# Kernel tuning notes

Measured on AMD Instinct MI355X. Metric: run time of the kernel, lower is better.

The kernel has to match this reference:

```python
import jax, jax.numpy as jnp
import numpy as np

K = 512          # patch size
H = 16           # heads
C = 768          # dim
ROPE_BASE = 100.0
COUNTS = [8000, 8300, 7800, 8668]


def _build_pad_unpad(counts, k):
    # faithful numpy replica of EfficientAttentionV2.get_padding_and_inverse
    counts = np.asarray(counts, dtype=np.int64)
    cpad = np.where(counts > k, ((counts + k - 1) // k) * k, counts)
    off = np.concatenate([[0], np.cumsum(counts)])
    offp = np.concatenate([[0], np.cumsum(cpad)])
    pad = np.arange(offp[-1])
    unpad = np.arange(off[-1])
    for i in range(len(counts)):
        unpad[off[i]:off[i + 1]] += offp[i] - off[i]
        if counts[i] != cpad[i]:
            s = offp[i + 1] - k + counts[i] % k
            pad[s:offp[i + 1]] = pad[s - k:offp[i + 1] - k]
        pad[offp[i]:offp[i + 1]] -= offp[i] - off[i]
    return pad, unpad


def setup_inputs() -> dict:
    key = jax.random.key(0)
    ks = jax.random.split(key, 6)
    N = int(np.sum(COUNTS))
    pad, unpad = _build_pad_unpad(COUNTS, K)
    rng = np.random.default_rng(0)
    perm = rng.permutation(N)                 # serialized_order stand-in
    inv_perm = np.argsort(perm)               # serialized_inverse
    order = perm[pad].astype(np.int32)        # [N_pad]
    inverse = unpad[inv_perm].astype(np.int32)  # [N]
    grid = rng.integers(0, 1024, size=(N, 3))
    pos = grid[order].astype(np.int32)        # [N_pad, 3], gathered grid coords
    s = 0.02
    return {
        "x": jax.random.normal(ks[0], (N, C), jnp.float32),
        "w_qkv": jax.random.normal(ks[1], (C, 3 * C), jnp.float32) * s,
        "b_qkv": jnp.zeros((3 * C,), jnp.float32),
        "w_proj": jax.random.normal(ks[2], (C, C), jnp.float32) * s,
        "b_proj": jnp.zeros((C,), jnp.float32),
        "order": jnp.asarray(order),
        "inverse": jnp.asarray(inverse),
        "pos": jnp.asarray(pos),
    }


def _rope1d(tok, pos1d):
    # tok: [P, K, H, d], pos1d: [P, K]
    d = tok.shape[-1]
    inv_freq = 1.0 / (ROPE_BASE ** (jnp.arange(0, d, 2, dtype=jnp.float32) / d))
    fr = pos1d[..., None].astype(jnp.float32) * inv_freq      # [P, K, d/2]
    fr = jnp.concatenate([fr, fr], axis=-1)[:, :, None, :]    # [P, K, 1, d]
    x1, x2 = jnp.split(tok, 2, axis=-1)
    rot = jnp.concatenate([-x2, x1], axis=-1)
    return tok * jnp.cos(fr) + rot * jnp.sin(fr)


def _rope3d(tok, pos):
    # tok: [P, K, H, D]; pos: [P, K, 3]; split head dim into 3 axis chunks
    parts = jnp.split(tok, 3, axis=-1)
    return jnp.concatenate(
        [_rope1d(parts[i], pos[..., i]) for i in range(3)], axis=-1)


def reference(x, w_qkv, b_qkv, w_proj, b_proj, order, inverse, pos):
    D = C // H
    scale = D ** -0.5
    qkv = x @ w_qkv + b_qkv                     # [N, 3C]
    qkv = qkv[order]                            # [N_pad, 3C] patch gather
    qkv = qkv.reshape(-1, K, 3, H, D)           # [P, K, 3, H, D]
    q, k, v = qkv[:, :, 0], qkv[:, :, 1], qkv[:, :, 2]  # [P, K, H, D]
    ppos = pos.reshape(-1, K, 3)
    q = _rope3d(q, ppos)
    k = _rope3d(k, ppos)
    attn = jnp.einsum("pkhd,pmhd->phkm", q, k) * scale
    attn = jax.nn.softmax(attn, axis=-1)
    feat = jnp.einsum("phkm,pmhd->pkhd", attn, v).reshape(-1, C)  # [N_pad, C]
    feat = feat[inverse]                        # [N, C] scatter-back
    return feat @ w_proj + b_proj
```

## Files before the change

### kernel.cpp

```cpp
#include <hip/hip_runtime.h>
#include <hip/hip_bf16.h>
#include <stdint.h>

typedef short short8 __attribute__((ext_vector_type(8)));
typedef short short4v __attribute__((ext_vector_type(4)));
typedef float f32x4 __attribute__((ext_vector_type(4)));
typedef float f32x16 __attribute__((ext_vector_type(16)));

#define AS1C(p) ((const __attribute__((address_space(1))) unsigned int*)(p))
#define AS3(p)  ((__attribute__((address_space(3))) unsigned int*)(p))

__device__ __forceinline__ short f2bf(float f) {
  union { float f; unsigned u; } v; v.f = f;
  unsigned r = v.u + 0x7FFFu + ((v.u >> 16) & 1u);
  return (short)(r >> 16);
}

__global__ void k_cast_bf16(const float* __restrict__ src, short* __restrict__ dst, int n8) {
  const int i = blockIdx.x * 256 + threadIdx.x;
  if (i >= n8) return;
  const float4* s = (const float4*)src + (size_t)i * 2;
  const float4 a = s[0], b = s[1];
  short8 o;
  o[0] = f2bf(a.x); o[1] = f2bf(a.y); o[2] = f2bf(a.z); o[3] = f2bf(a.w);
  o[4] = f2bf(b.x); o[5] = f2bf(b.y); o[6] = f2bf(b.z); o[7] = f2bf(b.w);
  ((short8*)dst)[i] = o;
}

__global__ void k_transpose_cast(const float* __restrict__ src, short* __restrict__ dst,
                                 int R, int C) {
  __shared__ float t[32][33];
  const int tx = threadIdx.x & 31, ty = threadIdx.x >> 5;
  const int c0 = blockIdx.x * 32, r0 = blockIdx.y * 32;
#pragma unroll
  for (int j = 0; j < 4; ++j)
    t[ty + j * 8][tx] = src[(size_t)(r0 + ty + j * 8) * C + c0 + tx];
  __syncthreads();
#pragma unroll
  for (int j = 0; j < 4; ++j)
    dst[(size_t)(c0 + ty + j * 8) * R + r0 + tx] = f2bf(t[tx][ty + j * 8]);
}

__global__ __launch_bounds__(256, 2)
void k_gemm1(const short* __restrict__ x16, const short* __restrict__ wt,
             const float* __restrict__ bqkv, const int* __restrict__ order,
             const int* __restrict__ pos,
             short* __restrict__ Qp, short* __restrict__ Kp, short* __restrict__ VpT) {
  __shared__ short sA[128 * 64];
  __shared__ short sB[128 * 64];
  __shared__ int sOrd[128];

  const int tid = threadIdx.x;
  const int lane = tid & 63;
  const int wv = tid >> 6;
  const int wm = wv >> 1, wn = wv & 1;
  const int tm = blockIdx.x * 128;
  const int tn = blockIdx.y * 128;

  if (tid < 128) sOrd[tid] = order[tm + tid];
  __syncthreads();

  const char* srcA[4];
  const char* srcB[4];
  {
    const int rr = tid >> 3, ck = tid & 7;
    const int sc = (ck ^ (rr & 7)) * 16;
#pragma unroll
    for (int is = 0; is < 4; ++is) {
      srcA[is] = (const char*)(x16 + (size_t)sOrd[is * 32 + rr] * 768) + sc;
      srcB[is] = (const char*)(wt + (size_t)(tn + is * 32 + rr) * 768) + sc;
    }
  }

  f32x4 acc[4][4] = {};
  const int ldsw = wv << 10;

  for (int kk = 0; kk < 12; ++kk) {
    const int kb = kk << 7;
#pragma unroll
    for (int is = 0; is < 4; ++is)
      __builtin_amdgcn_global_load_lds(AS1C(srcA[is] + kb), AS3((char*)sA + is * 4096 + ldsw), 16, 0, 0);
#pragma unroll
    for (int is = 0; is < 4; ++is)
      __builtin_amdgcn_global_load_lds(AS1C(srcB[is] + kb), AS3((char*)sB + is * 4096 + ldsw), 16, 0, 0);
    __syncthreads();

#pragma unroll
    for (int kbl = 0; kbl < 2; ++kbl) {
      const int ko = kbl * 64 + ((lane >> 4) << 4);
      short8 af[4], bf[4];
#pragma unroll
      for (int mi = 0; mi < 4; ++mi) {
        int row = wm * 64 + mi * 16 + (lane & 15);
        af[mi] = *(const short8*)((const char*)sA + row * 128 + (ko ^ ((row & 7) << 4)));
      }
#pragma unroll
      for (int ni = 0; ni < 4; ++ni) {
        int row = wn * 64 + ni * 16 + (lane & 15);
        bf[ni] = *(const short8*)((const char*)sB + row * 128 + (ko ^ ((row & 7) << 4)));
      }
#pragma unroll
      for (int mi = 0; mi < 4; ++mi)
#pragma unroll
        for (int ni = 0; ni < 4; ++ni)
          acc[mi][ni] = __builtin_amdgcn_mfma_f32_16x16x32_bf16(af[mi], bf[ni], acc[mi][ni], 0, 0, 0);
    }
    __syncthreads();
  }

  const int which = tn / 768;
  if (which == 2) {
#pragma unroll
    for (int ni = 0; ni < 4; ++ni) {
      const int col = tn + wn * 64 + ni * 16 + (lane & 15);
      const int hcol = col - 1536;
      const int h = hcol / 48;
      const int dd = hcol % 48;
      const float bq = bqkv[col];
#pragma unroll
      for (int mi = 0; mi < 4; ++mi) {
        const int m0 = tm + wm * 64 + mi * 16 + ((lane >> 4) << 2);
        const int p = m0 >> 9, q0 = m0 & 511;
        short4v vv;
#pragma unroll
        for (int r = 0; r < 4; ++r) vv[r] = f2bf(acc[mi][ni][r] + bq);
        *(short4v*)(VpT + ((size_t)(p * 16 + h) * 48 + dd) * 512 + q0) = vv;
      }
    }
  } else {
    const float invf = exp2f(-(float)(lane & 7) * 0.830482023721840f);
#pragma unroll
    for (int ni = 0; ni < 4; ++ni) {
      const int col = tn + wn * 64 + ni * 16 + (lane & 15);
      const int hcol = col - which * 768;
      const int h = hcol / 48;
      const int dd = hcol % 48;
      const int part = dd >> 4;
      const float bq = bqkv[col];
#pragma unroll
      for (int mi = 0; mi < 4; ++mi) {
        const int m0 = tm + wm * 64 + mi * 16 + ((lane >> 4) << 2);
#pragma unroll
        for (int r = 0; r < 4; ++r) {
          const int m = m0 + r;
          float val = acc[mi][ni][r] + bq;
          const int pv = pos[m * 3 + part];
          float s, c;
          __sincosf((float)pv * invf, &s, &c);
          const float partner = __shfl_xor(val, 8);
          val = val * c + ((lane & 8) ? partner : -partner) * s;
          const int p = m >> 9, q = m & 511;
          const size_t ro = (size_t)(p * 16 + h) * 512 + q;
          if (which == 0) Qp[ro * 48 + dd] = f2bf(val);
          else            Kp[(ro << 6) + dd] = f2bf(val);
        }
      }
    }
  }
}

__global__ __launch_bounds__(512, 2)
void k_attn(const short* __restrict__ Qp, const short* __restrict__ Kp,
            const short* __restrict__ VpT, short* __restrict__ featp) {
  __shared__ short sK[2][64 * 64];
  __shared__ short sV[2][64 * 64];

  const int tid = threadIdx.x;
  const int lane = tid & 63;
  const int wv = tid >> 6;
  const int l31 = lane & 31;
  const int hi = lane >> 5;
  const int ph = blockIdx.x;
  const int p = ph >> 4, h = ph & 15;

  ((float*)((char*)sV[0] + 6144))[tid] = 0.0f;
  ((float*)((char*)sV[1] + 6144))[tid] = 0.0f;

  short8 qf[2][3];
  {
    const short* Qb = Qp + ((size_t)ph * 512 + wv * 64) * 48;
#pragma unroll
    for (int qt = 0; qt < 2; ++qt)
#pragma unroll
      for (int dk = 0; dk < 3; ++dk)
        qf[qt][dk] = *(const short8*)(Qb + (qt * 32 + l31) * 48 + dk * 16 + hi * 8);
  }

  const char* Kb = (const char*)Kp + (size_t)ph * 65536;
  const char* Vb = (const char*)VpT + (size_t)ph * 49152;
  const int ldsw = wv << 10;
  const int o = tid * 16;
  const int swK = o ^ ((o >> 3) & 0x70);
  const int dV = tid >> 3;
  const int inrowV = (o & 127) ^ ((o >> 3) & 0x70);

  auto stage = [&](int b, int ms) {
    __builtin_amdgcn_global_load_lds(AS1C(Kb + ms * 8192 + swK), AS3((char*)sK[b] + ldsw), 16, 0, 0);
    if (tid < 384)
      __builtin_amdgcn_global_load_lds(AS1C(Vb + (size_t)dV * 1024 + ms * 128 + inrowV),
                                       AS3((char*)sV[b] + ldsw), 16, 0, 0);
  };

  stage(0, 0);
  asm volatile("s_waitcnt vmcnt(0)" ::: "memory");
  __syncthreads();

  f32x16 O[2][2] = {};
  float lr[2] = {0.f, 0.f};
  const float K2 = 0.14433756729740644f * 1.4426950408889634f;
  const float MB = 8.0f * K2;

  for (int ms = 0; ms < 8; ++ms) {
    const int bb = ms & 1;
    if (ms < 7) stage(bb ^ 1, ms + 1);

    const char* kb = (const char*)sK[bb];
    const char* vb = (const char*)sV[bb];

    f32x16 st[2][2];
    {
      short8 kf[2][3];
#pragma unroll
      for (int mt = 0; mt < 2; ++mt) {
        const int row = mt * 32 + l31;
        const int swr = (row & 7) << 4;
#pragma unroll
        for (int dk = 0; dk < 3; ++dk) {
          const int ob = (dk * 16 + hi * 8) * 2;
          kf[mt][dk] = *(const short8*)(kb + row * 128 + (ob ^ swr));
        }
      }
      __builtin_amdgcn_s_setprio(1);
#pragma unroll
      for (int mt = 0; mt < 2; ++mt)
#pragma unroll
        for (int qt = 0; qt < 2; ++qt) {
          f32x16 a = {};
#pragma unroll
          for (int dk = 0; dk < 3; ++dk)
            a = __builtin_amdgcn_mfma_f32_32x32x16_bf16(kf[mt][dk], qf[qt][dk], a, 0, 0, 0);
          st[mt][qt] = a;
        }
      __builtin_amdgcn_s_setprio(0);
    }

    unsigned pk[2][2][8];
#pragma unroll
    for (int qt = 0; qt < 2; ++qt) {
      float ps0 = 0.f, ps1 = 0.f;
#pragma unroll
      for (int mt = 0; mt < 2; ++mt) {
#pragma unroll
        for (int pr = 0; pr < 8; ++pr) {
          float p0 = __builtin_amdgcn_exp2f(st[mt][qt][pr * 2]     * K2 - MB);
          float p1 = __builtin_amdgcn_exp2f(st[mt][qt][pr * 2 + 1] * K2 - MB);
          ps0 += p0; ps1 += p1;
          __hip_bfloat162 bb2 = __float22bfloat162_rn(make_float2(p0, p1));
          unsigned w; __builtin_memcpy(&w, &bb2, 4);
          pk[mt][qt][pr] = w;
        }
      }
      lr[qt] += ps0 + ps1;
    }

    short8 vf[2][4];
#pragma unroll
    for (int dt = 0; dt < 2; ++dt) {
      const int d = dt * 32 + l31;
      const int swr = (d & 7) << 4;
#pragma unroll
      for (int ks = 0; ks < 4; ++ks) {
        const int ob = (ks * 16 + hi * 8) * 2;
        vf[dt][ks] = *(const short8*)(vb + d * 128 + (ob ^ swr));
      }
    }
#pragma unroll
    for (int qt = 0; qt < 2; ++qt) {
#pragma unroll
      for (int ks = 0; ks < 4; ++ks) {
        const int mt = ks >> 1;
        const int b0 = (ks & 1) * 4;
        const unsigned X0 = pk[mt][qt][b0 + 0];
        const unsigned X1 = pk[mt][qt][b0 + 1];
        const unsigned Y0 = pk[mt][qt][b0 + 2];
        const unsigned Y1 = pk[mt][qt][b0 + 3];
        const unsigned tX0 = __shfl_xor(X0, 32);
        const unsigned tX1 = __shfl_xor(X1, 32);
        const unsigned tY0 = __shfl_xor(Y0, 32);
        const unsigned tY1 = __shfl_xor(Y1, 32);
        union { unsigned u[4]; short8 v; } aw;
        aw.u[0] = hi ? tY0 : X0;
        aw.u[1] = hi ? tY1 : X1;
        aw.u[2] = hi ? Y0 : tX0;
        aw.u[3] = hi ? Y1 : tX1;
        __builtin_amdgcn_s_setprio(1);
#pragma unroll
        for (int dt = 0; dt < 2; ++dt)
          O[qt][dt] = __builtin_amdgcn_mfma_f32_32x32x16_bf16(aw.v, vf[dt][ks], O[qt][dt], 0, 0, 0);
        __builtin_amdgcn_s_setprio(0);
      }
    }

    if (ms < 7) {
      asm volatile("s_waitcnt vmcnt(0)" ::: "memory");
      __syncthreads();
    }
  }

#pragma unroll
  for (int qt = 0; qt < 2; ++qt) {
    float l = lr[qt] + __shfl_xor(lr[qt], 32);
    const float il = 1.0f / l;
#pragma unroll
    for (int r = 0; r < 16; ++r) {
      const int crow = (r & 3) + ((r >> 2) << 3) + (hi << 2);
      const float ilr = __shfl(il, crow);
      const int qg = wv * 64 + qt * 32 + crow;
      const size_t base = ((size_t)(p * 512 + qg)) * 768 + h * 48;
      featp[base + l31] = f2bf(O[qt][0][r] * ilr);
      if (l31 < 16) featp[base + 32 + l31] = f2bf(O[qt][1][r] * ilr);
    }
  }
}

__global__ __launch_bounds__(256, 2)
void k_gemm2(const short* __restrict__ featp, const short* __restrict__ wt,
             const float* __restrict__ bproj, const int* __restrict__ inverse,
             float* __restrict__ out) {
  __shared__ short sA[128 * 64];
  __shared__ short sB[128 * 64];
  __shared__ int sInv[128];

  const int tid = threadIdx.x;
  const int lane = tid & 63;
  const int wv = tid >> 6;
  const int wm = wv >> 1, wn = wv & 1;
  const int tm = blockIdx.x * 128;
  const int tn = blockIdx.y * 128;

  if (tid < 128) sInv[tid] = inverse[tm + tid];
  __syncthreads();

  const char* srcA[4];
  const char* srcB[4];
  {
    const int rr = tid >> 3, ck = tid & 7;
    const int sc = (ck ^ (rr & 7)) * 16;
#pragma unroll
    for (int is = 0; is < 4; ++is) {
      srcA[is] = (const char*)(featp + (size_t)sInv[is * 32 + rr] * 768) + sc;
      srcB[is] = (const char*)(wt + (size_t)(tn + is * 32 + rr) * 768) + sc;
    }
  }

  f32x4 acc[4][4] = {};
  const int ldsw = wv << 10;

  for (int kk = 0; kk < 12; ++kk) {
    const int kb = kk << 7;
#pragma unroll
    for (int is = 0; is < 4; ++is)
      __builtin_amdgcn_global_load_lds(AS1C(srcA[is] + kb), AS3((char*)sA + is * 4096 + ldsw), 16, 0, 0);
#pragma unroll
    for (int is = 0; is < 4; ++is)
      __builtin_amdgcn_global_load_lds(AS1C(srcB[is] + kb), AS3((char*)sB + is * 4096 + ldsw), 16, 0, 0);
    __syncthreads();

#pragma unroll
    for (int kbl = 0; kbl < 2; ++kbl) {
      const int ko = kbl * 64 + ((lane >> 4) << 4);
      short8 af[4], bf[4];
#pragma unroll
      for (int mi = 0; mi < 4; ++mi) {
        int row = wm * 64 + mi * 16 + (lane & 15);
        af[mi] = *(const short8*)((const char*)sA + row * 128 + (ko ^ ((row & 7) << 4)));
      }
#pragma unroll
      for (int ni = 0; ni < 4; ++ni) {
        int row = wn * 64 + ni * 16 + (lane & 15);
        bf[ni] = *(const short8*)((const char*)sB + row * 128 + (ko ^ ((row & 7) << 4)));
      }
#pragma unroll
      for (int mi = 0; mi < 4; ++mi)
#pragma unroll
        for (int ni = 0; ni < 4; ++ni)
          acc[mi][ni] = __builtin_amdgcn_mfma_f32_16x16x32_bf16(af[mi], bf[ni], acc[mi][ni], 0, 0, 0);
    }
    __syncthreads();
  }

#pragma unroll
  for (int ni = 0; ni < 4; ++ni) {
    const int col = tn + wn * 64 + ni * 16 + (lane & 15);
    const float bq = bproj[col];
#pragma unroll
    for (int mi = 0; mi < 4; ++mi) {
      const int m0 = tm + wm * 64 + mi * 16 + ((lane >> 4) << 2);
#pragma unroll
      for (int r = 0; r < 4; ++r)
        out[(size_t)(m0 + r) * 768 + col] = acc[mi][ni][r] + bq;
    }
  }
}

extern "C" void kernel_launch(void* const* d_in, const int* in_sizes, int n_in,
                              void* d_out, int out_size, void* d_ws, size_t ws_size,
                              hipStream_t stream) {
  (void)n_in; (void)out_size; (void)ws_size;
  const float* x      = (const float*)d_in[0];
  const float* w_qkv  = (const float*)d_in[1];
  const float* b_qkv  = (const float*)d_in[2];
  const float* w_proj = (const float*)d_in[3];
  const float* b_proj = (const float*)d_in[4];
  const int* order    = (const int*)d_in[5];
  const int* inverse  = (const int*)d_in[6];
  const int* pos      = (const int*)d_in[7];
  float* out = (float*)d_out;

  const int N = in_sizes[6];
  const int Npad = in_sizes[5];

  char* ws = (char*)d_ws;
  const size_t szTok = (size_t)Npad * 768 * 2;
  short* x16   = (short*)ws;
  short* featp = (short*)ws;
  short* wt1 = (short*)(ws + szTok);
  short* wt2 = (short*)(ws + szTok + 3538944);
  short* Qp  = (short*)(ws + szTok + 3538944 + 1179648);
  short* Kp  = (short*)(ws + szTok * 2 + 3538944 + 1179648);
  short* VpT = (short*)(ws + szTok * 2 + 3538944 + 1179648 + (size_t)Npad * 2048);

  k_cast_bf16<<<dim3((N * 768 / 8 + 255) / 256), 256, 0, stream>>>(x, x16, N * 768 / 8);
  k_transpose_cast<<<dim3(2304 / 32, 768 / 32), 256, 0, stream>>>(w_qkv, wt1, 768, 2304);
  k_transpose_cast<<<dim3(768 / 32, 768 / 32), 256, 0, stream>>>(w_proj, wt2, 768, 768);
  k_gemm1<<<dim3(Npad / 128, 18), 256, 0, stream>>>(x16, wt1, b_qkv, order, pos, Qp, Kp, VpT);
  k_attn<<<dim3((Npad / 512) * 16), 512, 0, stream>>>(Qp, Kp, VpT, featp);
  k_gemm2<<<dim3(N / 128, 6), 256, 0, stream>>>(featp, wt2, b_proj, inverse, out);
}
```

Measured before the change: 407.3 us.

## Split attention blocks into two 256-thread halves per patch-head

Each (patch, head) attention block of 512 threads is split into two 256-thread blocks, each handling half of the queries. This doubles the grid, which should improve load balance across CUs and raise occupancy (launch bounds go to 3 blocks per SM). The K/V staging is rewritten so fewer threads cover the same tiles, and the zero-fill of the LDS padding now writes float2. In exchange, K and V tiles are loaded from global memory twice, once by each half-block.

```diff
diff --git a/kernel.cpp b/kernel.cpp
--- a/kernel.cpp
+++ b/kernel.cpp
@@ -159,7 +159,7 @@
   }
 }
 
-__global__ __launch_bounds__(512, 2)
+__global__ __launch_bounds__(256, 3)
 void k_attn(const short* __restrict__ Qp, const short* __restrict__ Kp,
             const short* __restrict__ VpT, short* __restrict__ featp) {
   __shared__ short sK[2][64 * 64];
@@ -170,15 +170,17 @@
   const int wv = tid >> 6;
   const int l31 = lane & 31;
   const int hi = lane >> 5;
-  const int ph = blockIdx.x;
+  const int bid = blockIdx.x;
+  const int ph = bid >> 1;
+  const int half = bid & 1;
   const int p = ph >> 4, h = ph & 15;
 
-  ((float*)((char*)sV[0] + 6144))[tid] = 0.0f;
-  ((float*)((char*)sV[1] + 6144))[tid] = 0.0f;
+  ((float2*)((char*)sV[0] + 6144))[tid] = make_float2(0.f, 0.f);
+  ((float2*)((char*)sV[1] + 6144))[tid] = make_float2(0.f, 0.f);
 
   short8 qf[2][3];
   {
-    const short* Qb = Qp + ((size_t)ph * 512 + wv * 64) * 48;
+    const short* Qb = Qp + ((size_t)ph * 512 + half * 256 + wv * 64) * 48;
 #pragma unroll
     for (int qt = 0; qt < 2; ++qt)
 #pragma unroll
@@ -189,16 +191,29 @@
   const char* Kb = (const char*)Kp + (size_t)ph * 65536;
   const char* Vb = (const char*)VpT + (size_t)ph * 49152;
   const int ldsw = wv << 10;
-  const int o = tid * 16;
-  const int swK = o ^ ((o >> 3) & 0x70);
-  const int dV = tid >> 3;
-  const int inrowV = (o & 127) ^ ((o >> 3) & 0x70);
 
   auto stage = [&](int b, int ms) {
-    __builtin_amdgcn_global_load_lds(AS1C(Kb + ms * 8192 + swK), AS3((char*)sK[b] + ldsw), 16, 0, 0);
-    if (tid < 384)
-      __builtin_amdgcn_global_load_lds(AS1C(Vb + (size_t)dV * 1024 + ms * 128 + inrowV),
+#pragma unroll
+    for (int c = 0; c < 2; ++c) {
+      const int o2 = c * 4096 + tid * 16;
+      const int sw = o2 ^ ((o2 >> 3) & 0x70);
+      __builtin_amdgcn_global_load_lds(AS1C(Kb + ms * 8192 + sw),
+                                       AS3((char*)sK[b] + c * 4096 + ldsw), 16, 0, 0);
+    }
+    {
+      const int o2 = tid * 16;
+      const int d = o2 >> 7;
+      const int inrow = (o2 & 127) ^ ((o2 >> 3) & 0x70);
+      __builtin_amdgcn_global_load_lds(AS1C(Vb + (size_t)d * 1024 + ms * 128 + inrow),
                                        AS3((char*)sV[b] + ldsw), 16, 0, 0);
+    }
+    if (tid < 128) {
+      const int o2 = 4096 + tid * 16;
+      const int d = o2 >> 7;
+      const int inrow = (o2 & 127) ^ ((o2 >> 3) & 0x70);
+      __builtin_amdgcn_global_load_lds(AS1C(Vb + (size_t)d * 1024 + ms * 128 + inrow),
+                                       AS3((char*)sV[b] + 4096 + ldsw), 16, 0, 0);
+    }
   };
 
   stage(0, 0);
@@ -315,7 +330,7 @@
     for (int r = 0; r < 16; ++r) {
       const int crow = (r & 3) + ((r >> 2) << 3) + (hi << 2);
       const float ilr = __shfl(il, crow);
-      const int qg = wv * 64 + qt * 32 + crow;
+      const int qg = half * 256 + wv * 64 + qt * 32 + crow;
       const size_t base = ((size_t)(p * 512 + qg)) * 768 + h * 48;
       featp[base + l31] = f2bf(O[qt][0][r] * ilr);
       if (l31 < 16) featp[base + 32 + l31] = f2bf(O[qt][1][r] * ilr);
@@ -434,6 +449,6 @@
   k_transpose_cast<<<dim3(2304 / 32, 768 / 32), 256, 0, stream>>>(w_qkv, wt1, 768, 2304);
   k_transpose_cast<<<dim3(768 / 32, 768 / 32), 256, 0, stream>>>(w_proj, wt2, 768, 768);
   k_gemm1<<<dim3(Npad / 128, 18), 256, 0, stream>>>(x16, wt1, b_qkv, order, pos, Qp, Kp, VpT);
-  k_attn<<<dim3((Npad / 512) * 16), 512, 0, stream>>>(Qp, Kp, VpT, featp);
+  k_attn<<<dim3((Npad / 512) * 16 * 2), 256, 0, stream>>>(Qp, Kp, VpT, featp);
   k_gemm2<<<dim3(N / 128, 6), 256, 0, stream>>>(featp, wt2, b_proj, inverse, out);
 }
```

Measured after the change: 702.0 us. +72.4%, slower.
